# Kernel tuning notes

Measured on AMD Instinct MI355X. Metric: run time of the kernel, lower is better.

## Reference

```python
import jax, jax.numpy as jnp
import numpy as np

K_BITS = 4
V_BITS = 4
GROUP_SIZE = 64
EPS = 1e-8


def _quant_dequant_per_token(x, bits):
    # TurboQuantProd: symmetric per-token (per head_dim vector) absmax quantization.
    qmax = 2.0 ** (bits - 1) - 1.0
    scale = jnp.maximum(jnp.max(jnp.abs(x), axis=-1, keepdims=True) / qmax, EPS)
    return jnp.clip(jnp.round(x / scale), -qmax, qmax) * scale


def _quant_dequant_grouped(x, bits, group_size):
    # TurboQuantValue: symmetric grouped absmax quantization along head_dim.
    shp = x.shape
    xg = x.reshape(shp[:-1] + (shp[-1] // group_size, group_size))
    qmax = 2.0 ** (bits - 1) - 1.0
    scale = jnp.maximum(jnp.max(jnp.abs(xg), axis=-1, keepdims=True) / qmax, EPS)
    dq = jnp.clip(jnp.round(xg / scale), -qmax, qmax) * scale
    return dq.reshape(shp)


def setup_inputs() -> dict:
    key = jax.random.key(0)
    kq, kk, kv = jax.random.split(key, 3)
    B, H, S, D = 2, 16, 2048, 128
    query = jax.random.normal(kq, (B, H, S, D), dtype=jnp.float32)
    k = jax.random.normal(kk, (B, H, S, D), dtype=jnp.float32)
    v = jax.random.normal(kv, (B, H, S, D), dtype=jnp.float32)
    causal_mask = jnp.tril(jnp.ones((S, S), dtype=bool))[None, None]  # [1,1,S,S]
    return {"query": query, "key": k, "value": v, "causal_mask": causal_mask}


def reference(query, key, value, causal_mask):
    # Non-protected path: quantize K per-token, V grouped, then fused dequant + SDPA.
    head_dim = query.shape[-1]
    scale = 1.0 / np.sqrt(head_dim).astype(np.float32)
    dq_key = _quant_dequant_per_token(key, K_BITS)
    dq_value = _quant_dequant_grouped(value, V_BITS, GROUP_SIZE)
    scores = jnp.einsum('bhqd,bhkd->bhqk', query, dq_key) * scale
    scores = jnp.where(causal_mask, scores, -jnp.inf)
    weights = jax.nn.softmax(scores, axis=-1)
    output = jnp.einsum('bhqk,bhkd->bhqd', weights, dq_value)
    return (output, weights)
```

## Files before the change

kernel.cpp:

```cpp
#include <hip/hip_runtime.h>

#define SQ 2048
#define DD 128
#define BHN 32
#define SC2 0.12751741934f

typedef __attribute__((ext_vector_type(8))) short bf16x8;
typedef __attribute__((ext_vector_type(4))) float f32x4;

__device__ __forceinline__ unsigned short f2bf(float x){
  unsigned int u = __float_as_uint(x);
  unsigned int r = (u + 0x7FFFu + ((u >> 16) & 1u)) >> 16;
  return (unsigned short)r;
}
__device__ __forceinline__ unsigned pack2bf(float a, float b){
  return (unsigned)f2bf(a) | ((unsigned)f2bf(b) << 16);
}

__device__ __forceinline__ void gl_lds16(const void* g, void* l){
  __builtin_amdgcn_global_load_lds(
      (const __attribute__((address_space(1))) unsigned int*)g,
      (__attribute__((address_space(3))) unsigned int*)l, 16, 0, 0);
}

__global__ __launch_bounds__(256) void qd_kernel(const float* __restrict__ K,
                                                 const float* __restrict__ V,
                                                 char* __restrict__ dqK,
                                                 char* __restrict__ dqVt){
  __shared__ float Vlds[128*65];
  const int t = threadIdx.x;
  const int bh = blockIdx.x >> 5;
  const int stile = blockIdx.x & 31;
  const int tt = t >> 2;
  const int q4 = t & 3;
  const int s = stile*64 + tt;
  const long ebase = ((long)(bh*SQ + s))*DD + 32*q4;

  float vals[32];
  {
    const float4* kp = (const float4*)(K + ebase);
    float am = 0.f;
    #pragma unroll
    for (int j=0;j<8;j++){
      float4 v4 = kp[j];
      vals[4*j+0]=v4.x; vals[4*j+1]=v4.y; vals[4*j+2]=v4.z; vals[4*j+3]=v4.w;
      am = fmaxf(am, fmaxf(fmaxf(fabsf(v4.x),fabsf(v4.y)),fmaxf(fabsf(v4.z),fabsf(v4.w))));
    }
    am = fmaxf(am, __shfl_xor(am,1));
    am = fmaxf(am, __shfl_xor(am,2));
    const float sc = fmaxf(am/7.0f, 1e-8f);
    #pragma unroll
    for (int j=0;j<32;j++){
      float qv = rintf(vals[j]/sc);
      qv = fminf(7.f, fmaxf(-7.f, qv));
      vals[j] = qv*sc;
    }
    const long rowb = ((long)(bh*SQ + s))*256;
    const int swz = (s & 7) << 4;
    #pragma unroll
    for (int c=0;c<4;c++){
      uint4 w;
      w.x = pack2bf(vals[8*c+0], vals[8*c+1]);
      w.y = pack2bf(vals[8*c+2], vals[8*c+3]);
      w.z = pack2bf(vals[8*c+4], vals[8*c+5]);
      w.w = pack2bf(vals[8*c+6], vals[8*c+7]);
      *(uint4*)(dqK + rowb + ((64*q4 + 16*c) ^ swz)) = w;
    }
  }
  {
    const float4* vp = (const float4*)(V + ebase);
    float am = 0.f;
    #pragma unroll
    for (int j=0;j<8;j++){
      float4 v4 = vp[j];
      vals[4*j+0]=v4.x; vals[4*j+1]=v4.y; vals[4*j+2]=v4.z; vals[4*j+3]=v4.w;
      am = fmaxf(am, fmaxf(fmaxf(fabsf(v4.x),fabsf(v4.y)),fmaxf(fabsf(v4.z),fabsf(v4.w))));
    }
    am = fmaxf(am, __shfl_xor(am,1));
    const float sc = fmaxf(am/7.0f, 1e-8f);
    #pragma unroll
    for (int j=0;j<32;j++){
      float qv = rintf(vals[j]/sc);
      qv = fminf(7.f, fmaxf(-7.f, qv));
      Vlds[(32*q4 + j)*65 + tt] = qv*sc;
    }
  }
  __syncthreads();
  #pragma unroll
  for (int m=0;m<4;m++){
    const int chunk = m*256 + t;
    const int d = chunk >> 3;
    const int c = chunk & 7;
    uint4 w;
    const float* f = &Vlds[d*65 + 8*c];
    w.x = pack2bf(f[0], f[1]);
    w.y = pack2bf(f[2], f[3]);
    w.z = pack2bf(f[4], f[5]);
    w.w = pack2bf(f[6], f[7]);
    const long ob = ((long)(bh*DD + d))*4096 + (long)stile*128 + ((16*c) ^ ((d&7)<<4));
    *(uint4*)(dqVt + ob) = w;
  }
}

__global__ __launch_bounds__(256,2) void attn_fused(const float* __restrict__ Q,
    const char* __restrict__ dqK, const char* __restrict__ dqVt,
    float* __restrict__ Out, float* __restrict__ Wout){
  __shared__ __attribute__((aligned(16))) char Kt[2][16384];
  __shared__ __attribute__((aligned(16))) char Vt[2][16384];
  __shared__ __attribute__((aligned(16))) char Et[4][4096];

  const int bid = blockIdx.x;
  const int xcd = bid & 7;
  const int loc = bid >> 3;
  const int bh  = xcd*4 + (loc & 3);
  const int i   = loc >> 2;
  const int p   = (i < 8) ? i : (23 - i);
  const int t = threadIdx.x;
  const int lane = t & 63;
  const int w = t >> 6;
  const int l15 = lane & 15, l4 = lane >> 4;
  const int swz = (l15 & 7) << 4;

  const int qtA = 31 - p, qtB = p;
  const int q0A = qtA*64, q0B = qtB*64;
  const int nktA = qtA + 1;
  const int nktB = qtB + 1;
  const int rA = q0A + 16*w + l15;
  const int rB = q0B + 16*w + l15;

  bf16x8 qa[2][4];
  #pragma unroll
  for (int g=0; g<2; ++g){
    const int qrow = g ? rB : rA;
    const float* qb = Q + ((long)(bh*SQ) + qrow)*DD + 8*l4;
    #pragma unroll
    for (int kk=0;kk<4;kk++){
      float4 a = *(const float4*)(qb + 32*kk);
      float4 b = *(const float4*)(qb + 32*kk + 4);
      bf16x8 r;
      r[0]=(short)f2bf(a.x); r[1]=(short)f2bf(a.y); r[2]=(short)f2bf(a.z); r[3]=(short)f2bf(a.w);
      r[4]=(short)f2bf(b.x); r[5]=(short)f2bf(b.y); r[6]=(short)f2bf(b.z); r[7]=(short)f2bf(b.w);
      qa[g][kk]=r;
    }
  }

  const char* Kb = dqK + (long)bh*SQ*256;
  const char* Vb = dqVt + (long)bh*DD*4096;

  const f32x4 z4 = {0.f,0.f,0.f,0.f};
  f32x4 oacc[2][8] = {{z4,z4,z4,z4,z4,z4,z4,z4},{z4,z4,z4,z4,z4,z4,z4,z4}};
  float ssum[2] = {0.f, 0.f};
  char* eb = &Et[w][0];

  auto stageKV = [&](int buf, int kt){
    const char* ks = Kb + (long)kt*16384;
    #pragma unroll
    for (int it=0;it<4;it++)
      gl_lds16(ks + it*4096 + t*16, &Kt[buf][it*4096 + t*16]);
    const char* vs = Vb + (long)kt*128;
    #pragma unroll
    for (int it=0;it<4;it++)
      gl_lds16(vs + (long)(it*32 + (t>>3))*4096 + (t&7)*16, &Vt[buf][it*4096 + t*16]);
  };

  stageKV(0, 0);
  __syncthreads();
  int cur = 0;
  for (int kt=0; kt<nktA; ++kt){
    if (kt+1 < nktA) stageKV(cur^1, kt+1);
    const bool doB = (kt < nktB);
    const int k0 = kt*64;

    f32x4 sacc[2][4] = {{z4,z4,z4,z4},{z4,z4,z4,z4}};
    {
      const char* kbase = &Kt[cur][0] + l15*256;
      __builtin_amdgcn_s_setprio(1);
      if (doB){
        #pragma unroll
        for (int cf=0;cf<4;cf++){
          #pragma unroll
          for (int kk=0;kk<4;kk++){
            bf16x8 kb = *(const bf16x8*)(kbase + cf*4096 + ((64*kk+16*l4) ^ swz));
            sacc[0][cf] = __builtin_amdgcn_mfma_f32_16x16x32_bf16(kb, qa[0][kk], sacc[0][cf], 0,0,0);
            sacc[1][cf] = __builtin_amdgcn_mfma_f32_16x16x32_bf16(kb, qa[1][kk], sacc[1][cf], 0,0,0);
          }
        }
      } else {
        #pragma unroll
        for (int cf=0;cf<4;cf++){
          #pragma unroll
          for (int kk=0;kk<4;kk++){
            bf16x8 kb = *(const bf16x8*)(kbase + cf*4096 + ((64*kk+16*l4) ^ swz));
            sacc[0][cf] = __builtin_amdgcn_mfma_f32_16x16x32_bf16(kb, qa[0][kk], sacc[0][cf], 0,0,0);
          }
        }
      }
      __builtin_amdgcn_s_setprio(0);
    }

    {
      if (kt < qtA){
        #pragma unroll
        for (int cf=0;cf<4;cf++){
          float e0 = exp2f(sacc[0][cf][0]*SC2);
          float e1 = exp2f(sacc[0][cf][1]*SC2);
          float e2 = exp2f(sacc[0][cf][2]*SC2);
          float e3 = exp2f(sacc[0][cf][3]*SC2);
          ssum[0] += (e0+e1) + (e2+e3);
          uint2 wp; wp.x = pack2bf(e0,e1); wp.y = pack2bf(e2,e3);
          *(uint2*)(eb + l15*128 + ((32*cf + 8*l4) ^ swz)) = wp;
        }
      } else {
        #pragma unroll
        for (int cf=0;cf<4;cf++){
          const int tok0 = k0 + 16*cf + 4*l4;
          float e0 = (tok0+0 <= rA) ? exp2f(sacc[0][cf][0]*SC2) : 0.f;
          float e1 = (tok0+1 <= rA) ? exp2f(sacc[0][cf][1]*SC2) : 0.f;
          float e2 = (tok0+2 <= rA) ? exp2f(sacc[0][cf][2]*SC2) : 0.f;
          float e3 = (tok0+3 <= rA) ? exp2f(sacc[0][cf][3]*SC2) : 0.f;
          ssum[0] += (e0+e1) + (e2+e3);
          uint2 wp; wp.x = pack2bf(e0,e1); wp.y = pack2bf(e2,e3);
          *(uint2*)(eb + l15*128 + ((32*cf + 8*l4) ^ swz)) = wp;
        }
      }
    }
    if (doB){
      const int lr = 16 + l15;
      if (kt < qtB){
        #pragma unroll
        for (int cf=0;cf<4;cf++){
          float e0 = exp2f(sacc[1][cf][0]*SC2);
          float e1 = exp2f(sacc[1][cf][1]*SC2);
          float e2 = exp2f(sacc[1][cf][2]*SC2);
          float e3 = exp2f(sacc[1][cf][3]*SC2);
          ssum[1] += (e0+e1) + (e2+e3);
          uint2 wp; wp.x = pack2bf(e0,e1); wp.y = pack2bf(e2,e3);
          *(uint2*)(eb + lr*128 + ((32*cf + 8*l4) ^ swz)) = wp;
        }
      } else {
        #pragma unroll
        for (int cf=0;cf<4;cf++){
          const int tok0 = k0 + 16*cf + 4*l4;
          float e0 = (tok0+0 <= rB) ? exp2f(sacc[1][cf][0]*SC2) : 0.f;
          float e1 = (tok0+1 <= rB) ? exp2f(sacc[1][cf][1]*SC2) : 0.f;
          float e2 = (tok0+2 <= rB) ? exp2f(sacc[1][cf][2]*SC2) : 0.f;
          float e3 = (tok0+3 <= rB) ? exp2f(sacc[1][cf][3]*SC2) : 0.f;
          ssum[1] += (e0+e1) + (e2+e3);
          uint2 wp; wp.x = pack2bf(e0,e1); wp.y = pack2bf(e2,e3);
          *(uint2*)(eb + lr*128 + ((32*cf + 8*l4) ^ swz)) = wp;
        }
      }
    }

    {
      const char* vbase = &Vt[cur][0] + l15*128;
      __builtin_amdgcn_s_setprio(1);
      if (doB){
        #pragma unroll
        for (int kc=0;kc<2;kc++){
          const int eo = (64*kc + 16*l4) ^ swz;
          bf16x8 ea0 = *(const bf16x8*)(eb + l15*128 + eo);
          bf16x8 ea1 = *(const bf16x8*)(eb + (16+l15)*128 + eo);
          #pragma unroll
          for (int df=0;df<8;df++){
            bf16x8 vv = *(const bf16x8*)(vbase + df*2048 + eo);
            oacc[0][df] = __builtin_amdgcn_mfma_f32_16x16x32_bf16(ea0, vv, oacc[0][df], 0,0,0);
            oacc[1][df] = __builtin_amdgcn_mfma_f32_16x16x32_bf16(ea1, vv, oacc[1][df], 0,0,0);
          }
        }
      } else {
        #pragma unroll
        for (int kc=0;kc<2;kc++){
          const int eo = (64*kc + 16*l4) ^ swz;
          bf16x8 ea0 = *(const bf16x8*)(eb + l15*128 + eo);
          #pragma unroll
          for (int df=0;df<8;df++){
            bf16x8 vv = *(const bf16x8*)(vbase + df*2048 + eo);
            oacc[0][df] = __builtin_amdgcn_mfma_f32_16x16x32_bf16(ea0, vv, oacc[0][df], 0,0,0);
          }
        }
      }
      __builtin_amdgcn_s_setprio(0);
    }
    __syncthreads();
    cur ^= 1;
  }

  float si[2];
  #pragma unroll
  for (int g=0; g<2; ++g){
    float sm = ssum[g];
    sm += __shfl_xor(sm, 16);
    sm += __shfl_xor(sm, 32);
    si[g] = 1.0f / sm;
    float invr[4];
    #pragma unroll
    for (int ii=0;ii<4;ii++) invr[ii] = __shfl(si[g], 4*l4+ii);
    const int rb0 = (g ? q0B : q0A) + 16*w;
    float* ob = Out + ((long)(bh*SQ) + rb0)*DD;
    #pragma unroll
    for (int df=0;df<8;df++){
      #pragma unroll
      for (int ii=0;ii<4;ii++)
        ob[(4*l4+ii)*DD + 16*df + l15] = oacc[g][df][ii]*invr[ii];
    }
  }

  float* Wbase = Wout + (long)bh*SQ*SQ;
  float* wrowA = Wbase + (long)rA*SQ;
  float* wrowB = Wbase + (long)rB*SQ;

  for (int kt=0; kt<nktA; ++kt){
    const int k0 = kt*64;
    const char* kr = Kb + (long)kt*16384 + l15*256;
    const bool doB = (kt < nktB);

    bf16x8 kb[4][4];
    #pragma unroll
    for (int cf=0;cf<4;cf++){
      #pragma unroll
      for (int kk=0;kk<4;kk++)
        kb[cf][kk] = *(const bf16x8*)(kr + cf*4096 + ((64*kk+16*l4) ^ swz));
    }

    f32x4 sacc[2][4] = {{z4,z4,z4,z4},{z4,z4,z4,z4}};
    __builtin_amdgcn_s_setprio(1);
    if (doB){
      #pragma unroll
      for (int cf=0;cf<4;cf++){
        #pragma unroll
        for (int kk=0;kk<4;kk++){
          sacc[0][cf] = __builtin_amdgcn_mfma_f32_16x16x32_bf16(kb[cf][kk], qa[0][kk], sacc[0][cf], 0,0,0);
          sacc[1][cf] = __builtin_amdgcn_mfma_f32_16x16x32_bf16(kb[cf][kk], qa[1][kk], sacc[1][cf], 0,0,0);
        }
      }
    } else {
      #pragma unroll
      for (int cf=0;cf<4;cf++){
        #pragma unroll
        for (int kk=0;kk<4;kk++)
          sacc[0][cf] = __builtin_amdgcn_mfma_f32_16x16x32_bf16(kb[cf][kk], qa[0][kk], sacc[0][cf], 0,0,0);
      }
    }
    __builtin_amdgcn_s_setprio(0);

    if (kt < qtA){
      #pragma unroll
      for (int cf=0;cf<4;cf++){
        const int tok0 = k0 + 16*cf + 4*l4;
        f32x4 wv;
        wv[0] = exp2f(sacc[0][cf][0]*SC2)*si[0];
        wv[1] = exp2f(sacc[0][cf][1]*SC2)*si[0];
        wv[2] = exp2f(sacc[0][cf][2]*SC2)*si[0];
        wv[3] = exp2f(sacc[0][cf][3]*SC2)*si[0];
        *(f32x4*)(wrowA + tok0) = wv;
      }
    } else {
      #pragma unroll
      for (int cf=0;cf<4;cf++){
        const int tok0 = k0 + 16*cf + 4*l4;
        f32x4 wv;
        wv[0] = (tok0+0 <= rA) ? exp2f(sacc[0][cf][0]*SC2)*si[0] : 0.f;
        wv[1] = (tok0+1 <= rA) ? exp2f(sacc[0][cf][1]*SC2)*si[0] : 0.f;
        wv[2] = (tok0+2 <= rA) ? exp2f(sacc[0][cf][2]*SC2)*si[0] : 0.f;
        wv[3] = (tok0+3 <= rA) ? exp2f(sacc[0][cf][3]*SC2)*si[0] : 0.f;
        *(f32x4*)(wrowA + tok0) = wv;
      }
    }
    if (doB){
      if (kt < qtB){
        #pragma unroll
        for (int cf=0;cf<4;cf++){
          const int tok0 = k0 + 16*cf + 4*l4;
          f32x4 wv;
          wv[0] = exp2f(sacc[1][cf][0]*SC2)*si[1];
          wv[1] = exp2f(sacc[1][cf][1]*SC2)*si[1];
          wv[2] = exp2f(sacc[1][cf][2]*SC2)*si[1];
          wv[3] = exp2f(sacc[1][cf][3]*SC2)*si[1];
          *(f32x4*)(wrowB + tok0) = wv;
        }
      } else {
        #pragma unroll
        for (int cf=0;cf<4;cf++){
          const int tok0 = k0 + 16*cf + 4*l4;
          f32x4 wv;
          wv[0] = (tok0+0 <= rB) ? exp2f(sacc[1][cf][0]*SC2)*si[1] : 0.f;
          wv[1] = (tok0+1 <= rB) ? exp2f(sacc[1][cf][1]*SC2)*si[1] : 0.f;
          wv[2] = (tok0+2 <= rB) ? exp2f(sacc[1][cf][2]*SC2)*si[1] : 0.f;
          wv[3] = (tok0+3 <= rB) ? exp2f(sacc[1][cf][3]*SC2)*si[1] : 0.f;
          *(f32x4*)(wrowB + tok0) = wv;
        }
      }
    }
  }

  const f32x4 zz = {0.f,0.f,0.f,0.f};
  {
    const int z0 = nktA*64;
    for (int rr=0; rr<16 && z0 < SQ; rr++){
      float* row = Wbase + (long)(q0A + 16*w + rr)*SQ;
      for (int c = z0 + 4*lane; c < SQ; c += 256)
        *(f32x4*)(row + c) = zz;
    }
  }
  {
    const int z0 = nktB*64;
    for (int rr=0; rr<16; rr++){
      float* row = Wbase + (long)(q0B + 16*w + rr)*SQ;
      for (int c = z0 + 4*lane; c < SQ; c += 256)
        *(f32x4*)(row + c) = zz;
    }
  }
}

extern "C" void kernel_launch(void* const* d_in, const int* in_sizes, int n_in,
                              void* d_out, int out_size, void* d_ws, size_t ws_size,
                              hipStream_t stream) {
  const float* Q = (const float*)d_in[0];
  const float* K = (const float*)d_in[1];
  const float* V = (const float*)d_in[2];
  float* Out = (float*)d_out;
  float* Wout = (float*)d_out + (size_t)BHN*SQ*DD;
  char* dqK  = (char*)d_ws;
  char* dqVt = (char*)d_ws + (size_t)BHN*SQ*DD*2;

  qd_kernel<<<BHN*32, 256, 0, stream>>>(K, V, dqK, dqVt);
  attn_fused<<<512, 256, 0, stream>>>(Q, dqK, dqVt, Out, Wout);
}
```

Baseline: 232.7 us.

## Overlap row-B weight recomputation and writes with the row-A main loop

```diff
diff --git a/kernel.cpp b/kernel.cpp
--- a/kernel.cpp
+++ b/kernel.cpp
@@ -146,10 +146,14 @@
 
   const char* Kb = dqK + (long)bh*SQ*256;
   const char* Vb = dqVt + (long)bh*DD*4096;
+  float* Wbase = Wout + (long)bh*SQ*SQ;
+  float* wrowA = Wbase + (long)rA*SQ;
+  float* wrowB = Wbase + (long)rB*SQ;
 
   const f32x4 z4 = {0.f,0.f,0.f,0.f};
   f32x4 oacc[2][8] = {{z4,z4,z4,z4,z4,z4,z4,z4},{z4,z4,z4,z4,z4,z4,z4,z4}};
   float ssum[2] = {0.f, 0.f};
+  float si1 = 0.f;
   char* eb = &Et[w][0];
 
   auto stageKV = [&](int buf, int kt){
@@ -171,6 +175,25 @@
     const bool doB = (kt < nktB);
     const int k0 = kt*64;
 
+    if (kt == nktB){
+      float sm = ssum[1];
+      sm += __shfl_xor(sm, 16);
+      sm += __shfl_xor(sm, 32);
+      si1 = 1.0f / sm;
+    }
+    const int kt2 = kt - nktB;
+    const bool doB2 = (!doB) && (kt2 < nktB);
+    bf16x8 kb2[4][4];
+    if (doB2){
+      const char* kr = Kb + (long)kt2*16384 + l15*256;
+      #pragma unroll
+      for (int cf=0;cf<4;cf++){
+        #pragma unroll
+        for (int kk=0;kk<4;kk++)
+          kb2[cf][kk] = *(const bf16x8*)(kr + cf*4096 + ((64*kk+16*l4) ^ swz));
+      }
+    }
+
     f32x4 sacc[2][4] = {{z4,z4,z4,z4},{z4,z4,z4,z4}};
     {
       const char* kbase = &Kt[cur][0] + l15*256;
@@ -196,6 +219,41 @@
         }
       }
       __builtin_amdgcn_s_setprio(0);
+    }
+
+    if (doB2){
+      const int k0b = kt2*64;
+      if (kt2 < qtB){
+        #pragma unroll
+        for (int cf=0;cf<4;cf++){
+          f32x4 sb = z4;
+          #pragma unroll
+          for (int kk=0;kk<4;kk++)
+            sb = __builtin_amdgcn_mfma_f32_16x16x32_bf16(kb2[cf][kk], qa[1][kk], sb, 0,0,0);
+          const int tok0 = k0b + 16*cf + 4*l4;
+          f32x4 wv;
+          wv[0] = exp2f(sb[0]*SC2)*si1;
+          wv[1] = exp2f(sb[1]*SC2)*si1;
+          wv[2] = exp2f(sb[2]*SC2)*si1;
+          wv[3] = exp2f(sb[3]*SC2)*si1;
+          *(f32x4*)(wrowB + tok0) = wv;
+        }
+      } else {
+        #pragma unroll
+        for (int cf=0;cf<4;cf++){
+          f32x4 sb = z4;
+          #pragma unroll
+          for (int kk=0;kk<4;kk++)
+            sb = __builtin_amdgcn_mfma_f32_16x16x32_bf16(kb2[cf][kk], qa[1][kk], sb, 0,0,0);
+          const int tok0 = k0b + 16*cf + 4*l4;
+          f32x4 wv;
+          wv[0] = (tok0+0 <= rB) ? exp2f(sb[0]*SC2)*si1 : 0.f;
+          wv[1] = (tok0+1 <= rB) ? exp2f(sb[1]*SC2)*si1 : 0.f;
+          wv[2] = (tok0+2 <= rB) ? exp2f(sb[2]*SC2)*si1 : 0.f;
+          wv[3] = (tok0+3 <= rB) ? exp2f(sb[3]*SC2)*si1 : 0.f;
+          *(f32x4*)(wrowB + tok0) = wv;
+        }
+      }
     }
 
     {
@@ -286,16 +344,19 @@
     cur ^= 1;
   }
 
-  float si[2];
+  float si0;
+  {
+    float sm = ssum[0];
+    sm += __shfl_xor(sm, 16);
+    sm += __shfl_xor(sm, 32);
+    si0 = 1.0f / sm;
+  }
   #pragma unroll
   for (int g=0; g<2; ++g){
-    float sm = ssum[g];
-    sm += __shfl_xor(sm, 16);
-    sm += __shfl_xor(sm, 32);
-    si[g] = 1.0f / sm;
+    const float sg = g ? si1 : si0;
     float invr[4];
     #pragma unroll
-    for (int ii=0;ii<4;ii++) invr[ii] = __shfl(si[g], 4*l4+ii);
+    for (int ii=0;ii<4;ii++) invr[ii] = __shfl(sg, 4*l4+ii);
     const int rb0 = (g ? q0B : q0A) + 16*w;
     float* ob = Out + ((long)(bh*SQ) + rb0)*DD;
     #pragma unroll
@@ -306,14 +367,52 @@
     }
   }
 
-  float* Wbase = Wout + (long)bh*SQ*SQ;
-  float* wrowA = Wbase + (long)rA*SQ;
-  float* wrowB = Wbase + (long)rB*SQ;
+  for (int kt2 = nktA - nktB; kt2 < nktB; ++kt2){
+    const char* kr = Kb + (long)kt2*16384 + l15*256;
+    bf16x8 kb2[4][4];
+    #pragma unroll
+    for (int cf=0;cf<4;cf++){
+      #pragma unroll
+      for (int kk=0;kk<4;kk++)
+        kb2[cf][kk] = *(const bf16x8*)(kr + cf*4096 + ((64*kk+16*l4) ^ swz));
+    }
+    const int k0b = kt2*64;
+    if (kt2 < qtB){
+      #pragma unroll
+      for (int cf=0;cf<4;cf++){
+        f32x4 sb = z4;
+        #pragma unroll
+        for (int kk=0;kk<4;kk++)
+          sb = __builtin_amdgcn_mfma_f32_16x16x32_bf16(kb2[cf][kk], qa[1][kk], sb, 0,0,0);
+        const int tok0 = k0b + 16*cf + 4*l4;
+        f32x4 wv;
+        wv[0] = exp2f(sb[0]*SC2)*si1;
+        wv[1] = exp2f(sb[1]*SC2)*si1;
+        wv[2] = exp2f(sb[2]*SC2)*si1;
+        wv[3] = exp2f(sb[3]*SC2)*si1;
+        *(f32x4*)(wrowB + tok0) = wv;
+      }
+    } else {
+      #pragma unroll
+      for (int cf=0;cf<4;cf++){
+        f32x4 sb = z4;
+        #pragma unroll
+        for (int kk=0;kk<4;kk++)
+          sb = __builtin_amdgcn_mfma_f32_16x16x32_bf16(kb2[cf][kk], qa[1][kk], sb, 0,0,0);
+        const int tok0 = k0b + 16*cf + 4*l4;
+        f32x4 wv;
+        wv[0] = (tok0+0 <= rB) ? exp2f(sb[0]*SC2)*si1 : 0.f;
+        wv[1] = (tok0+1 <= rB) ? exp2f(sb[1]*SC2)*si1 : 0.f;
+        wv[2] = (tok0+2 <= rB) ? exp2f(sb[2]*SC2)*si1 : 0.f;
+        wv[3] = (tok0+3 <= rB) ? exp2f(sb[3]*SC2)*si1 : 0.f;
+        *(f32x4*)(wrowB + tok0) = wv;
+      }
+    }
+  }
 
   for (int kt=0; kt<nktA; ++kt){
     const int k0 = kt*64;
     const char* kr = Kb + (long)kt*16384 + l15*256;
-    const bool doB = (kt < nktB);
 
     bf16x8 kb[4][4];
     #pragma unroll
@@ -323,24 +422,13 @@
         kb[cf][kk] = *(const bf16x8*)(kr + cf*4096 + ((64*kk+16*l4) ^ swz));
     }
 
-    f32x4 sacc[2][4] = {{z4,z4,z4,z4},{z4,z4,z4,z4}};
+    f32x4 sacc[4] = {z4,z4,z4,z4};
     __builtin_amdgcn_s_setprio(1);
-    if (doB){
-      #pragma unroll
-      for (int cf=0;cf<4;cf++){
-        #pragma unroll
-        for (int kk=0;kk<4;kk++){
-          sacc[0][cf] = __builtin_amdgcn_mfma_f32_16x16x32_bf16(kb[cf][kk], qa[0][kk], sacc[0][cf], 0,0,0);
-          sacc[1][cf] = __builtin_amdgcn_mfma_f32_16x16x32_bf16(kb[cf][kk], qa[1][kk], sacc[1][cf], 0,0,0);
-        }
-      }
-    } else {
-      #pragma unroll
-      for (int cf=0;cf<4;cf++){
-        #pragma unroll
-        for (int kk=0;kk<4;kk++)
-          sacc[0][cf] = __builtin_amdgcn_mfma_f32_16x16x32_bf16(kb[cf][kk], qa[0][kk], sacc[0][cf], 0,0,0);
-      }
+    #pragma unroll
+    for (int cf=0;cf<4;cf++){
+      #pragma unroll
+      for (int kk=0;kk<4;kk++)
+        sacc[cf] = __builtin_amdgcn_mfma_f32_16x16x32_bf16(kb[cf][kk], qa[0][kk], sacc[cf], 0,0,0);
     }
     __builtin_amdgcn_s_setprio(0);
 
@@ -349,10 +437,10 @@
       for (int cf=0;cf<4;cf++){
         const int tok0 = k0 + 16*cf + 4*l4;
         f32x4 wv;
-        wv[0] = exp2f(sacc[0][cf][0]*SC2)*si[0];
-        wv[1] = exp2f(sacc[0][cf][1]*SC2)*si[0];
-        wv[2] = exp2f(sacc[0][cf][2]*SC2)*si[0];
-        wv[3] = exp2f(sacc[0][cf][3]*SC2)*si[0];
+        wv[0] = exp2f(sacc[cf][0]*SC2)*si0;
+        wv[1] = exp2f(sacc[cf][1]*SC2)*si0;
+        wv[2] = exp2f(sacc[cf][2]*SC2)*si0;
+        wv[3] = exp2f(sacc[cf][3]*SC2)*si0;
         *(f32x4*)(wrowA + tok0) = wv;
       }
     } else {
@@ -360,36 +448,11 @@
       for (int cf=0;cf<4;cf++){
         const int tok0 = k0 + 16*cf + 4*l4;
         f32x4 wv;
-        wv[0] = (tok0+0 <= rA) ? exp2f(sacc[0][cf][0]*SC2)*si[0] : 0.f;
-        wv[1] = (tok0+1 <= rA) ? exp2f(sacc[0][cf][1]*SC2)*si[0] : 0.f;
-        wv[2] = (tok0+2 <= rA) ? exp2f(sacc[0][cf][2]*SC2)*si[0] : 0.f;
-        wv[3] = (tok0+3 <= rA) ? exp2f(sacc[0][cf][3]*SC2)*si[0] : 0.f;
+        wv[0] = (tok0+0 <= rA) ? exp2f(sacc[cf][0]*SC2)*si0 : 0.f;
+        wv[1] = (tok0+1 <= rA) ? exp2f(sacc[cf][1]*SC2)*si0 : 0.f;
+        wv[2] = (tok0+2 <= rA) ? exp2f(sacc[cf][2]*SC2)*si0 : 0.f;
+        wv[3] = (tok0+3 <= rA) ? exp2f(sacc[cf][3]*SC2)*si0 : 0.f;
         *(f32x4*)(wrowA + tok0) = wv;
-      }
-    }
-    if (doB){
-      if (kt < qtB){
-        #pragma unroll
-        for (int cf=0;cf<4;cf++){
-          const int tok0 = k0 + 16*cf + 4*l4;
-          f32x4 wv;
-          wv[0] = exp2f(sacc[1][cf][0]*SC2)*si[1];
-          wv[1] = exp2f(sacc[1][cf][1]*SC2)*si[1];
-          wv[2] = exp2f(sacc[1][cf][2]*SC2)*si[1];
-          wv[3] = exp2f(sacc[1][cf][3]*SC2)*si[1];
-          *(f32x4*)(wrowB + tok0) = wv;
-        }
-      } else {
-        #pragma unroll
-        for (int cf=0;cf<4;cf++){
-          const int tok0 = k0 + 16*cf + 4*l4;
-          f32x4 wv;
-          wv[0] = (tok0+0 <= rB) ? exp2f(sacc[1][cf][0]*SC2)*si[1] : 0.f;
-          wv[1] = (tok0+1 <= rB) ? exp2f(sacc[1][cf][1]*SC2)*si[1] : 0.f;
-          wv[2] = (tok0+2 <= rB) ? exp2f(sacc[1][cf][2]*SC2)*si[1] : 0.f;
-          wv[3] = (tok0+3 <= rB) ? exp2f(sacc[1][cf][3]*SC2)*si[1] : 0.f;
-          *(f32x4*)(wrowB + tok0) = wv;
-        }
       }
     }
   }
```

New measurement: 271.1 us. 1.17x slower.
